# Kernel optimization log

Hardware: AMD Instinct MI355X
Metric: run time of the kernel (lower is better)

The kernel has to match this reference:

```python
import jax, jax.numpy as jnp
import numpy as np

S, D, F = 4096, 1024, 4096
EPS = 1e-5

def _layernorm(x, g, b):
    mu = jnp.mean(x, axis=-1, keepdims=True)
    var = jnp.mean(jnp.square(x - mu), axis=-1, keepdims=True)
    return (x - mu) * jax.lax.rsqrt(var + EPS) * g + b

def setup_inputs() -> dict:
    key = jax.random.key(0)
    ks = jax.random.split(key, 16)
    s = 0.02
    inp = {
        "query": jax.random.normal(ks[0], (S, D), jnp.float32),
        "key":   jax.random.normal(ks[1], (S, D), jnp.float32),
        "value": jax.random.normal(ks[2], (S, D), jnp.float32),
        "mask":  jax.random.uniform(ks[3], (S, S), jnp.float32),
        # attention linears (stored [in, out]; y = x @ W + b)
        "Wq": jax.random.normal(ks[4], (D, D), jnp.float32) * s,
        "bq": jnp.zeros((D,), jnp.float32),
        "Wk": jax.random.normal(ks[5], (D, D), jnp.float32) * s,
        "bk": jnp.zeros((D,), jnp.float32),
        "Wv": jax.random.normal(ks[6], (D, D), jnp.float32) * s,
        "bv": jnp.zeros((D,), jnp.float32),
        "Wo": jax.random.normal(ks[7], (D, D), jnp.float32) * s,
        "bo": jnp.zeros((D,), jnp.float32),
        # layernorm 1
        "g1": jnp.ones((D,), jnp.float32),
        "be1": jnp.zeros((D,), jnp.float32),
        # feed forward
        "W1": jax.random.normal(ks[8], (D, F), jnp.float32) * s,
        "bf1": jnp.zeros((F,), jnp.float32),
        "W2": jax.random.normal(ks[9], (F, D), jnp.float32) * s,
        "bf2": jnp.zeros((D,), jnp.float32),
        # layernorm 2
        "g2": jnp.ones((D,), jnp.float32),
        "be2": jnp.zeros((D,), jnp.float32),
    }
    return inp

def reference(query, key, value, mask, Wq, bq, Wk, bk, Wv, bv, Wo, bo,
              g1, be1, W1, bf1, W2, bf2, g2, be2):
    q = query @ Wq + bq                      # [S, D]
    k = key @ Wk + bk                        # [S, D]
    v = value @ Wv + bv                      # [S, D]
    scores = q @ k.T                         # [S, S]
    masked = scores * mask                   # multiplicative mask
    h = jax.nn.softmax(masked / jnp.sqrt(jnp.float32(D)), axis=0)  # softmax over dim 0
    attn = (h @ v) @ Wo + bo                 # [S, D]
    # dropout is identity in eval mode
    n1 = _layernorm(attn + query, g1, be1)
    ff = jax.nn.relu(n1 @ W1 + bf1) @ W2 + bf2
    return _layernorm(ff + n1, g2, be2)
```

## Files before the change

### kernel.cpp

```cpp
#include <hip/hip_runtime.h>
#include <hip/hip_bf16.h>

#define S_DIM 4096
#define D_DIM 1024
#define F_DIM 4096

typedef unsigned short ushort_t;
typedef __attribute__((ext_vector_type(8))) short sh8;
typedef __attribute__((ext_vector_type(4))) short sh4;
typedef __attribute__((ext_vector_type(4))) float fx4;

__device__ __forceinline__ ushort_t f2bf(float f) {
    union { float f; unsigned u; } v; v.f = f;
    unsigned r = v.u + 0x7fffu + ((v.u >> 16) & 1u);
    return (ushort_t)(r >> 16);
}
__device__ __forceinline__ float bf2f(ushort_t u) {
    union { unsigned u; float f; } v; v.u = ((unsigned)u) << 16;
    return v.f;
}

typedef const __attribute__((address_space(1))) void* gvp;
typedef __attribute__((address_space(3))) void* svp;
__device__ __forceinline__ void gload_lds16(const void* g, void* l) {
    __builtin_amdgcn_global_load_lds((gvp)g, (svp)l, 16, 0, 0);
}

#define BM 128
#define BN 128
#define BK 32
#define LDS_BUF 16384

template<bool BIAS, bool RELU, bool SCALE, bool OUTBF, bool SPLITK>
__device__ __forceinline__
void gemm_body(const ushort_t* A, const ushort_t* Bt,
               const float* bias,
               float* Cf, ushort_t* Cb,
               int M, int N, int K, int kBeg, int kEnd, float scale)
{
    __shared__ ushort_t lds[3 * (BM * BK + BN * BK)];
    const int tid = threadIdx.x;
    const int bm = blockIdx.x, bn = blockIdx.y;
    const int w  = tid >> 6, l = tid & 63;
    const int wm = w >> 1, wn = w & 1;

    fx4 acc[4][4] = {};

    const ushort_t* Ag = A  + (size_t)(bm * BM) * K;
    const ushort_t* Bg = Bt + (size_t)(bn * BN) * K;

    const int srow = tid >> 2;
    const int scs  = (tid & 3) ^ (srow & 3);

    auto stage = [&](int b, int k0) {
        char* base = (char*)lds + b * LDS_BUF;
        #pragma unroll
        for (int c = 0; c < 2; ++c) {
            int row = c * 64 + srow;
            gload_lds16(Ag + (size_t)row * K + k0 + scs * 8,
                        base + c * 4096 + tid * 16);
            gload_lds16(Bg + (size_t)row * K + k0 + scs * 8,
                        base + 8192 + c * 4096 + tid * 16);
        }
    };

    const int nt = (kEnd - kBeg) / BK;

    stage(0, kBeg);
    if (nt > 1) {
        stage(1, kBeg + BK);
        asm volatile("s_waitcnt vmcnt(4)" ::: "memory");
    } else {
        asm volatile("s_waitcnt vmcnt(0)" ::: "memory");
    }
    __builtin_amdgcn_s_barrier();
    __builtin_amdgcn_sched_barrier(0);

    int cur = 0;
    for (int t = 0; t < nt; ++t) {
        int stg = cur + 2; if (stg >= 3) stg -= 3;
        if (t + 2 < nt) stage(stg, kBeg + (t + 2) * BK);

        char* lbase = (char*)lds + cur * LDS_BUF;
        sh8 af[4], bfr[4];
        #pragma unroll
        for (int q = 0; q < 4; ++q) {
            int ra = wm * 64 + q * 16 + (l & 15);
            int ca = (l >> 4) ^ (ra & 3);
            af[q]  = *(const sh8*)(lbase + ra * 64 + ca * 16);
            int rb = wn * 64 + q * 16 + (l & 15);
            int cb = (l >> 4) ^ (rb & 3);
            bfr[q] = *(const sh8*)(lbase + 8192 + rb * 64 + cb * 16);
        }
        #pragma unroll
        for (int i = 0; i < 4; ++i)
            #pragma unroll
            for (int j = 0; j < 4; ++j)
                acc[i][j] = __builtin_amdgcn_mfma_f32_16x16x32_bf16(
                                af[i], bfr[j], acc[i][j], 0, 0, 0);

        asm volatile("s_waitcnt lgkmcnt(0)" ::: "memory");
        if (t + 2 < nt)      asm volatile("s_waitcnt vmcnt(4)" ::: "memory");
        else if (t + 1 < nt) asm volatile("s_waitcnt vmcnt(0)" ::: "memory");
        if (t + 1 < nt) {
            __builtin_amdgcn_s_barrier();
            __builtin_amdgcn_sched_barrier(0);
        }
        cur = cur + 1; if (cur == 3) cur = 0;
    }

    if (SPLITK) Cb += (size_t)blockIdx.z * M * N;

    const int crow0 = bm * BM + wm * 64;
    const int ccol0 = bn * BN + wn * 64;
    #pragma unroll
    for (int i = 0; i < 4; ++i) {
        #pragma unroll
        for (int j = 0; j < 4; ++j) {
            int col = ccol0 + j * 16 + (l & 15);
            float bia = BIAS ? bias[col] : 0.f;
            #pragma unroll
            for (int r = 0; r < 4; ++r) {
                int row = crow0 + i * 16 + (l >> 4) * 4 + r;
                float v = acc[i][j][r] + bia;
                if (SCALE) v *= scale;
                if (RELU) v = fmaxf(v, 0.f);
                if (OUTBF) Cb[(size_t)row * N + col] = f2bf(v);
                else       Cf[(size_t)row * N + col] = v;
            }
        }
    }
}

template<bool BIAS, bool RELU, bool SCALE, bool OUTBF>
__global__ __launch_bounds__(256)
void gemm_bt(const ushort_t* __restrict__ A, const ushort_t* __restrict__ Bt,
             const float* __restrict__ bias,
             float* __restrict__ Cf, ushort_t* __restrict__ Cb,
             int M, int N, int K, float scale)
{
    gemm_body<BIAS, RELU, SCALE, OUTBF, false>(A, Bt, bias, Cf, Cb,
                                               M, N, K, 0, K, scale);
}

__global__ __launch_bounds__(256)
void gemm_bt_sk(const ushort_t* __restrict__ A, const ushort_t* __restrict__ Bt,
                ushort_t* __restrict__ Cpart, int M, int N, int K, int Ks)
{
    int z = blockIdx.z;
    gemm_body<false, false, false, true, true>(A, Bt, nullptr,
                                               nullptr, Cpart,
                                               M, N, K, z * Ks, z * Ks + Ks, 1.f);
}

__global__ __launch_bounds__(256)
void qkv_gemm(const ushort_t* qin, const ushort_t* kin, const ushort_t* vin,
              const ushort_t* WqT, const ushort_t* WkT, const ushort_t* WvT,
              const float* bq, const float* bk, const float* bv,
              ushort_t* qb, ushort_t* kb, ushort_t* vb, int M, int N, int K)
{
    const ushort_t* A; const ushort_t* Bt; const float* bias; ushort_t* C;
    if (blockIdx.z == 0)      { A = qin; Bt = WqT; bias = bq; C = qb; }
    else if (blockIdx.z == 1) { A = kin; Bt = WkT; bias = bk; C = kb; }
    else                      { A = vin; Bt = WvT; bias = bv; C = vb; }
    gemm_body<true, false, false, true, false>(A, Bt, bias,
                                               nullptr, C, M, N, K, 0, K, 1.f);
}

template<int NS>
__global__ __launch_bounds__(256)
void reduce_sk(const ushort_t* __restrict__ parts, ushort_t* __restrict__ ob,
               size_t MN)
{
    size_t idx = ((size_t)blockIdx.x * 256 + threadIdx.x) * 8;
    float s[8] = {0.f, 0.f, 0.f, 0.f, 0.f, 0.f, 0.f, 0.f};
    #pragma unroll
    for (int p = 0; p < NS; ++p) {
        sh8 v = *(const sh8*)(parts + (size_t)p * MN + idx);
        #pragma unroll
        for (int j = 0; j < 8; ++j) s[j] += bf2f((ushort_t)v[j]);
    }
    sh8 r;
    #pragma unroll
    for (int j = 0; j < 8; ++j) r[j] = (short)f2bf(s[j]);
    *(sh8*)(ob + idx) = r;
}

__global__ __launch_bounds__(256)
void transpose_f32_bf16(const float* __restrict__ in, ushort_t* __restrict__ out,
                        int R, int C)
{
    __shared__ float t[32][33];
    int bc = blockIdx.x * 32, br = blockIdx.y * 32;
    int tx = threadIdx.x & 31, ty = threadIdx.x >> 5;
    #pragma unroll
    for (int i = 0; i < 32; i += 8)
        t[ty + i][tx] = in[(size_t)(br + ty + i) * C + bc + tx];
    __syncthreads();
    #pragma unroll
    for (int i = 0; i < 32; i += 8)
        out[(size_t)(bc + ty + i) * R + br + tx] = f2bf(t[tx][ty + i]);
}

__global__ __launch_bounds__(256)
void transpose4_f32_bf16(const float* w0, const float* w1,
                         const float* w2, const float* w3,
                         ushort_t* o0, ushort_t* o1, ushort_t* o2, ushort_t* o3)
{
    const int R = D_DIM, C = D_DIM;
    const float* in; ushort_t* out;
    if (blockIdx.z == 0)      { in = w0; out = o0; }
    else if (blockIdx.z == 1) { in = w1; out = o1; }
    else if (blockIdx.z == 2) { in = w2; out = o2; }
    else                      { in = w3; out = o3; }
    __shared__ float t[32][33];
    int bc = blockIdx.x * 32, br = blockIdx.y * 32;
    int tx = threadIdx.x & 31, ty = threadIdx.x >> 5;
    #pragma unroll
    for (int i = 0; i < 32; i += 8)
        t[ty + i][tx] = in[(size_t)(br + ty + i) * C + bc + tx];
    __syncthreads();
    #pragma unroll
    for (int i = 0; i < 32; i += 8)
        out[(size_t)(bc + ty + i) * R + br + tx] = f2bf(t[tx][ty + i]);
}

__global__ __launch_bounds__(256)
void transpose_bf16(const ushort_t* __restrict__ in, ushort_t* __restrict__ out,
                    int R, int C)
{
    __shared__ ushort_t t[32][33];
    int bc = blockIdx.x * 32, br = blockIdx.y * 32;
    int tx = threadIdx.x & 31, ty = threadIdx.x >> 5;
    #pragma unroll
    for (int i = 0; i < 32; i += 8)
        t[ty + i][tx] = in[(size_t)(br + ty + i) * C + bc + tx];
    __syncthreads();
    #pragma unroll
    for (int i = 0; i < 32; i += 8)
        out[(size_t)(bc + ty + i) * R + br + tx] = t[tx][ty + i];
}

__global__ __launch_bounds__(256)
void cvt_bf16_3(const float* a, const float* b, const float* c,
                ushort_t* oa, ushort_t* ob, ushort_t* oc)
{
    const float* in; ushort_t* out;
    if (blockIdx.y == 0)      { in = a; out = oa; }
    else if (blockIdx.y == 1) { in = b; out = ob; }
    else                      { in = c; out = oc; }
    int i = (blockIdx.x * 256 + threadIdx.x) * 8;
    const float4* p = (const float4*)(in + i);
    float4 x = p[0], y = p[1];
    sh8 r;
    r[0] = (short)f2bf(x.x); r[1] = (short)f2bf(x.y);
    r[2] = (short)f2bf(x.z); r[3] = (short)f2bf(x.w);
    r[4] = (short)f2bf(y.x); r[5] = (short)f2bf(y.y);
    r[6] = (short)f2bf(y.z); r[7] = (short)f2bf(y.w);
    *(sh8*)(out + i) = r;
}

#define NCH 256
#define ROWS_PER_CH (S_DIM / NCH)

__global__ __launch_bounds__(256)
void smax_pass1(ushort_t* __restrict__ m, const float* __restrict__ mask,
                float* __restrict__ pmax, float* __restrict__ psum)
{
    int c0 = (blockIdx.x * 256 + threadIdx.x) * 8;
    int chunk = blockIdx.y;
    int r0 = chunk * ROWS_PER_CH;

    float mx[8], sm[8];
    #pragma unroll
    for (int j = 0; j < 8; ++j) { mx[j] = -1e30f; sm[j] = 0.f; }

    for (int i = 0; i < ROWS_PER_CH; ++i) {
        size_t off = (size_t)(r0 + i) * S_DIM + c0;
        sh8 mv = *(const sh8*)(m + off);
        float4 k0 = ((const float4*)(mask + off))[0];
        float4 k1 = ((const float4*)(mask + off))[1];
        float mk[8] = {k0.x, k0.y, k0.z, k0.w, k1.x, k1.y, k1.z, k1.w};
        sh8 wv;
        #pragma unroll
        for (int j = 0; j < 8; ++j) {
            float v0 = bf2f((ushort_t)mv[j]) * mk[j];
            ushort_t wb = f2bf(v0);
            wv[j] = (short)wb;
            float v = bf2f(wb);
            float nm = fmaxf(mx[j], v);
            sm[j] = sm[j] * __expf(mx[j] - nm) + __expf(v - nm);
            mx[j] = nm;
        }
        *(sh8*)(m + off) = wv;
    }
    #pragma unroll
    for (int j = 0; j < 8; ++j) {
        pmax[(size_t)(c0 + j) * NCH + chunk] = mx[j];
        psum[(size_t)(c0 + j) * NCH + chunk] = sm[j];
    }
}

__global__ __launch_bounds__(256)
void smax_pass2(const float* __restrict__ pmax, const float* __restrict__ psum,
                float* __restrict__ cmax, float* __restrict__ cinv)
{
    int col = blockIdx.x, t = threadIdx.x;
    float m = pmax[(size_t)col * NCH + t];
    float s = psum[(size_t)col * NCH + t];

    __shared__ float red[8];
    int w = t >> 6, l = t & 63;

    float mx = m;
    #pragma unroll
    for (int off = 32; off; off >>= 1) mx = fmaxf(mx, __shfl_down(mx, off));
    if (!l) red[w] = mx;
    __syncthreads();
    mx = fmaxf(fmaxf(red[0], red[1]), fmaxf(red[2], red[3]));
    __syncthreads();

    float sc = s * __expf(m - mx);
    #pragma unroll
    for (int off = 32; off; off >>= 1) sc += __shfl_down(sc, off);
    if (!l) red[4 + w] = sc;
    __syncthreads();
    if (t == 0) {
        float total = red[4] + red[5] + red[6] + red[7];
        cmax[col] = mx;
        cinv[col] = 1.f / total;
    }
}

__global__ __launch_bounds__(256)
void smax_pass3(const ushort_t* __restrict__ m,
                const float* __restrict__ cmax, const float* __restrict__ cinv,
                ushort_t* __restrict__ h)
{
    size_t idx = ((size_t)blockIdx.x * 256 + threadIdx.x) * 8;
    int col0 = (int)(idx & (S_DIM - 1));
    sh8 mv = *(const sh8*)(m + idx);
    sh8 r;
    #pragma unroll
    for (int j = 0; j < 8; ++j) {
        int c = col0 + j;
        float v = bf2f((ushort_t)mv[j]);
        r[j] = (short)f2bf(__expf(v - cmax[c]) * cinv[c]);
    }
    *(sh8*)(h + idx) = r;
}

template<int NS, bool WB>
__global__ __launch_bounds__(256)
void add_ln_sk(const ushort_t* __restrict__ parts, const float* __restrict__ pbias,
               const float* __restrict__ resid, const float* __restrict__ g,
               const float* __restrict__ be,
               float* __restrict__ of, ushort_t* __restrict__ ob)
{
    const int D = D_DIM;
    const size_t SD = (size_t)S_DIM * D_DIM;
    int row = blockIdx.x, tid = threadIdx.x;
    size_t base = (size_t)row * D + tid * 4;

    float4 vr = *(const float4*)(resid + base);
    float4 vbi = ((const float4*)pbias)[tid];
    float x0 = vr.x + vbi.x, x1 = vr.y + vbi.y, x2 = vr.z + vbi.z, x3 = vr.w + vbi.w;
    #pragma unroll
    for (int p = 0; p < NS; ++p) {
        sh4 v = *(const sh4*)(parts + p * SD + base);
        x0 += bf2f((ushort_t)v[0]); x1 += bf2f((ushort_t)v[1]);
        x2 += bf2f((ushort_t)v[2]); x3 += bf2f((ushort_t)v[3]);
    }

    float s = x0 + x1 + x2 + x3;
    float q = x0 * x0 + x1 * x1 + x2 * x2 + x3 * x3;
    #pragma unroll
    for (int off = 32; off; off >>= 1) {
        s += __shfl_down(s, off);
        q += __shfl_down(q, off);
    }
    __shared__ float red[8];
    int w = tid >> 6, l = tid & 63;
    if (!l) { red[w] = s; red[4 + w] = q; }
    __syncthreads();
    s = red[0] + red[1] + red[2] + red[3];
    q = red[4] + red[5] + red[6] + red[7];
    float mu = s * (1.f / D);
    float rstd = rsqrtf(q * (1.f / D) - mu * mu + 1e-5f);
    float4 vg  = ((const float4*)g)[tid];
    float4 vbe = ((const float4*)be)[tid];
    float y0 = (x0 - mu) * rstd * vg.x + vbe.x;
    float y1 = (x1 - mu) * rstd * vg.y + vbe.y;
    float y2 = (x2 - mu) * rstd * vg.z + vbe.z;
    float y3 = (x3 - mu) * rstd * vg.w + vbe.w;
    float4 r; r.x = y0; r.y = y1; r.z = y2; r.w = y3;
    *(float4*)(of + base) = r;
    if (WB) {
        sh4 rb;
        rb[0] = (short)f2bf(y0); rb[1] = (short)f2bf(y1);
        rb[2] = (short)f2bf(y2); rb[3] = (short)f2bf(y3);
        *(sh4*)(ob + base) = rb;
    }
}

extern "C" void kernel_launch(void* const* d_in, const int* in_sizes, int n_in,
                              void* d_out, int out_size, void* d_ws, size_t ws_size,
                              hipStream_t stream)
{
    const float* query = (const float*)d_in[0];
    const float* key_  = (const float*)d_in[1];
    const float* value = (const float*)d_in[2];
    const float* mask  = (const float*)d_in[3];
    const float* Wq = (const float*)d_in[4];  const float* bq = (const float*)d_in[5];
    const float* Wk = (const float*)d_in[6];  const float* bk = (const float*)d_in[7];
    const float* Wv = (const float*)d_in[8];  const float* bv = (const float*)d_in[9];
    const float* Wo = (const float*)d_in[10]; const float* bo = (const float*)d_in[11];
    const float* g1 = (const float*)d_in[12]; const float* be1 = (const float*)d_in[13];
    const float* W1 = (const float*)d_in[14]; const float* bf1 = (const float*)d_in[15];
    const float* W2 = (const float*)d_in[16]; const float* bf2 = (const float*)d_in[17];
    const float* g2 = (const float*)d_in[18]; const float* be2 = (const float*)d_in[19];

    const size_t MB = 1ull << 20;
    char* ws = (char*)d_ws;
    ushort_t* WqT = (ushort_t*)(ws);
    ushort_t* WkT = (ushort_t*)(ws + 2 * MB);
    ushort_t* WvT = (ushort_t*)(ws + 4 * MB);
    ushort_t* WoT = (ushort_t*)(ws + 6 * MB);
    ushort_t* W1T = (ushort_t*)(ws + 8 * MB);
    ushort_t* W2T = (ushort_t*)(ws + 16 * MB);
    ushort_t* qin = (ushort_t*)(ws + 24 * MB);
    ushort_t* kin = (ushort_t*)(ws + 32 * MB);
    ushort_t* vin = (ushort_t*)(ws + 40 * MB);
    ushort_t* qb  = (ushort_t*)(ws + 48 * MB);
    ushort_t* kb  = (ushort_t*)(ws + 56 * MB);
    ushort_t* vb  = (ushort_t*)(ws + 64 * MB);
    ushort_t* vT  = (ushort_t*)(ws + 72 * MB);
    ushort_t* msc = (ushort_t*)(ws + 80 * MB);
    ushort_t* hb  = (ushort_t*)(ws + 112 * MB);
    float*   pmax = (float*)(ws + 144 * MB);
    float*   psum = (float*)(ws + 148 * MB);
    float*   cmax = (float*)(ws + 152 * MB);
    float*   cinv = (float*)(ws + 152 * MB + 64 * 1024);
    ushort_t* pts1  = (ushort_t*)(ws + 80 * MB);
    ushort_t* apb   = (ushort_t*)(ws + 24 * MB);
    ushort_t* pts2  = (ushort_t*)(ws + 80 * MB);
    float*    n1f   = (float*)(ws + 48 * MB);
    ushort_t* n1b   = (ushort_t*)(ws + 64 * MB);
    ushort_t* mid   = (ushort_t*)(ws + 112 * MB);
    ushort_t* pts3  = (ushort_t*)(ws + 80 * MB);

    const int S = S_DIM, D = D_DIM, F = F_DIM;

    transpose4_f32_bf16<<<dim3(D / 32, D / 32, 4), 256, 0, stream>>>(
        Wq, Wk, Wv, Wo, WqT, WkT, WvT, WoT);
    transpose_f32_bf16<<<dim3(F / 32, D / 32), 256, 0, stream>>>(W1, W1T, D, F);
    transpose_f32_bf16<<<dim3(D / 32, F / 32), 256, 0, stream>>>(W2, W2T, F, D);

    cvt_bf16_3<<<dim3(S * D / 8 / 256, 3), 256, 0, stream>>>(
        query, key_, value, qin, kin, vin);

    qkv_gemm<<<dim3(S / BM, D / BN, 3), 256, 0, stream>>>(
        qin, kin, vin, WqT, WkT, WvT, bq, bk, bv, qb, kb, vb, S, D, D);

    transpose_bf16<<<dim3(D / 32, S / 32), 256, 0, stream>>>(vb, vT, S, D);

    gemm_bt<false, false, true, true><<<dim3(S / BM, S / BN), 256, 0, stream>>>(
        qb, kb, nullptr, nullptr, msc, S, S, D, 0.03125f);

    smax_pass1<<<dim3(S / 2048, NCH), 256, 0, stream>>>(msc, mask, pmax, psum);
    smax_pass2<<<S, 256, 0, stream>>>(pmax, psum, cmax, cinv);
    smax_pass3<<<(size_t)S * S / 8 / 256, 256, 0, stream>>>(msc, cmax, cinv, hb);

    gemm_bt_sk<<<dim3(S / BM, D / BN, 4), 256, 0, stream>>>(hb, vT, pts1, S, D, S, S / 4);
    reduce_sk<4><<<S * D / 2048, 256, 0, stream>>>(pts1, apb, (size_t)S * D);

    gemm_bt_sk<<<dim3(S / BM, D / BN, 2), 256, 0, stream>>>(apb, WoT, pts2, S, D, D, D / 2);

    add_ln_sk<2, true><<<S, 256, 0, stream>>>(pts2, bo, query, g1, be1, n1f, n1b);

    gemm_bt<true, true, false, true><<<dim3(S / BM, F / BN), 256, 0, stream>>>(
        n1b, W1T, bf1, nullptr, mid, S, F, D, 1.f);

    gemm_bt_sk<<<dim3(S / BM, D / BN, 4), 256, 0, stream>>>(mid, W2T, pts3, S, D, F, F / 4);

    add_ln_sk<4, false><<<S, 256, 0, stream>>>(pts3, bf2, n1f, g2, be2,
                                               (float*)d_out, nullptr);
}
```

Measured before the change: 358.6 us.

## Add 256x256-tile 512-thread GEMM and use it for the large matmuls

```diff
diff --git a/kernel.cpp b/kernel.cpp
--- a/kernel.cpp
+++ b/kernel.cpp
@@ -165,6 +165,132 @@
     else                      { A = vin; Bt = WvT; bias = bv; C = vb; }
     gemm_body<true, false, false, true, false>(A, Bt, bias,
                                                nullptr, C, M, N, K, 0, K, 1.f);
+}
+
+#define G2_BM 256
+#define G2_BN 256
+#define G2_BUF 32768
+
+template<bool BIAS, bool RELU, bool SCALE, bool OUTBF, bool SPLITK>
+__device__ __forceinline__
+void gemm256_body(const ushort_t* A, const ushort_t* Bt,
+                  const float* bias,
+                  float* Cf, ushort_t* Cb,
+                  int M, int N, int K, int kBeg, int kEnd, float scale)
+{
+    __shared__ ushort_t lds[3 * (G2_BM * BK + G2_BN * BK)];
+    const int tid = threadIdx.x;
+    const int bm = blockIdx.x, bn = blockIdx.y;
+    const int w  = tid >> 6, l = tid & 63;
+    const int wm = w >> 2, wn = w & 3;
+
+    fx4 acc[8][4] = {};
+
+    const ushort_t* Ag = A  + (size_t)(bm * G2_BM) * K;
+    const ushort_t* Bg = Bt + (size_t)(bn * G2_BN) * K;
+
+    auto stage = [&](int b, int k0) {
+        char* base = (char*)lds + b * G2_BUF;
+        #pragma unroll
+        for (int c = 0; c < 2; ++c) {
+            int idx = c * 512 + tid;
+            int row = idx >> 2;
+            int cs  = idx & 3;
+            gload_lds16(Ag + (size_t)row * K + k0 + cs * 8,
+                        base + idx * 16);
+            gload_lds16(Bg + (size_t)row * K + k0 + cs * 8,
+                        base + 16384 + idx * 16);
+        }
+    };
+
+    const int nt = (kEnd - kBeg) / BK;
+
+    stage(0, kBeg);
+    if (nt > 1) {
+        stage(1, kBeg + BK);
+        asm volatile("s_waitcnt vmcnt(4)" ::: "memory");
+    } else {
+        asm volatile("s_waitcnt vmcnt(0)" ::: "memory");
+    }
+    __builtin_amdgcn_s_barrier();
+    __builtin_amdgcn_sched_barrier(0);
+
+    int cur = 0;
+    for (int t = 0; t < nt; ++t) {
+        int stg = cur + 2; if (stg >= 3) stg -= 3;
+        if (t + 2 < nt) stage(stg, kBeg + (t + 2) * BK);
+
+        char* lbase = (char*)lds + cur * G2_BUF;
+        sh8 af[8], bfr[4];
+        #pragma unroll
+        for (int q = 0; q < 8; ++q) {
+            int ra = wm * 128 + q * 16 + (l & 15);
+            af[q] = *(const sh8*)(lbase + ra * 64 + (l >> 4) * 16);
+        }
+        #pragma unroll
+        for (int j = 0; j < 4; ++j) {
+            int rb = wn * 64 + j * 16 + (l & 15);
+            bfr[j] = *(const sh8*)(lbase + 16384 + rb * 64 + (l >> 4) * 16);
+        }
+        #pragma unroll
+        for (int i = 0; i < 8; ++i)
+            #pragma unroll
+            for (int j = 0; j < 4; ++j)
+                acc[i][j] = __builtin_amdgcn_mfma_f32_16x16x32_bf16(
+                                af[i], bfr[j], acc[i][j], 0, 0, 0);
+
+        asm volatile("s_waitcnt lgkmcnt(0)" ::: "memory");
+        if (t + 2 < nt)      asm volatile("s_waitcnt vmcnt(4)" ::: "memory");
+        else if (t + 1 < nt) asm volatile("s_waitcnt vmcnt(0)" ::: "memory");
+        if (t + 1 < nt) {
+            __builtin_amdgcn_s_barrier();
+            __builtin_amdgcn_sched_barrier(0);
+        }
+        cur = cur + 1; if (cur == 3) cur = 0;
+    }
+
+    if (SPLITK) Cb += (size_t)blockIdx.z * M * N;
+
+    const int crow0 = bm * G2_BM + wm * 128;
+    const int ccol0 = bn * G2_BN + wn * 64;
+    #pragma unroll
+    for (int i = 0; i < 8; ++i) {
+        #pragma unroll
+        for (int j = 0; j < 4; ++j) {
+            int col = ccol0 + j * 16 + (l & 15);
+            float bia = BIAS ? bias[col] : 0.f;
+            #pragma unroll
+            for (int r = 0; r < 4; ++r) {
+                int row = crow0 + i * 16 + (l >> 4) * 4 + r;
+                float v = acc[i][j][r] + bia;
+                if (SCALE) v *= scale;
+                if (RELU) v = fmaxf(v, 0.f);
+                if (OUTBF) Cb[(size_t)row * N + col] = f2bf(v);
+                else       Cf[(size_t)row * N + col] = v;
+            }
+        }
+    }
+}
+
+template<bool BIAS, bool RELU, bool SCALE, bool OUTBF>
+__global__ __launch_bounds__(512)
+void gemm256_bt(const ushort_t* __restrict__ A, const ushort_t* __restrict__ Bt,
+                const float* __restrict__ bias,
+                float* __restrict__ Cf, ushort_t* __restrict__ Cb,
+                int M, int N, int K, float scale)
+{
+    gemm256_body<BIAS, RELU, SCALE, OUTBF, false>(A, Bt, bias, Cf, Cb,
+                                                  M, N, K, 0, K, scale);
+}
+
+__global__ __launch_bounds__(512)
+void gemm256_bt_sk(const ushort_t* __restrict__ A, const ushort_t* __restrict__ Bt,
+                   ushort_t* __restrict__ Cpart, int M, int N, int K, int Ks)
+{
+    int z = blockIdx.z;
+    gemm256_body<false, false, false, true, true>(A, Bt, nullptr,
+                                                  nullptr, Cpart,
+                                                  M, N, K, z * Ks, z * Ks + Ks, 1.f);
 }
 
 template<int NS>
@@ -464,24 +590,26 @@
 
     transpose_bf16<<<dim3(D / 32, S / 32), 256, 0, stream>>>(vb, vT, S, D);
 
-    gemm_bt<false, false, true, true><<<dim3(S / BM, S / BN), 256, 0, stream>>>(
+    gemm256_bt<false, false, true, true><<<dim3(S / G2_BM, S / G2_BN), 512, 0, stream>>>(
         qb, kb, nullptr, nullptr, msc, S, S, D, 0.03125f);
 
     smax_pass1<<<dim3(S / 2048, NCH), 256, 0, stream>>>(msc, mask, pmax, psum);
     smax_pass2<<<S, 256, 0, stream>>>(pmax, psum, cmax, cinv);
     smax_pass3<<<(size_t)S * S / 8 / 256, 256, 0, stream>>>(msc, cmax, cinv, hb);
 
-    gemm_bt_sk<<<dim3(S / BM, D / BN, 4), 256, 0, stream>>>(hb, vT, pts1, S, D, S, S / 4);
+    gemm256_bt_sk<<<dim3(S / G2_BM, D / G2_BN, 4), 512, 0, stream>>>(
+        hb, vT, pts1, S, D, S, S / 4);
     reduce_sk<4><<<S * D / 2048, 256, 0, stream>>>(pts1, apb, (size_t)S * D);
 
     gemm_bt_sk<<<dim3(S / BM, D / BN, 2), 256, 0, stream>>>(apb, WoT, pts2, S, D, D, D / 2);
 
     add_ln_sk<2, true><<<S, 256, 0, stream>>>(pts2, bo, query, g1, be1, n1f, n1b);
 
-    gemm_bt<true, true, false, true><<<dim3(S / BM, F / BN), 256, 0, stream>>>(
+    gemm256_bt<true, true, false, true><<<dim3(S / G2_BM, F / G2_BN), 512, 0, stream>>>(
         n1b, W1T, bf1, nullptr, mid, S, F, D, 1.f);
 
-    gemm_bt_sk<<<dim3(S / BM, D / BN, 4), 256, 0, stream>>>(mid, W2T, pts3, S, D, F, F / 4);
+    gemm256_bt_sk<<<dim3(S / G2_BM, D / G2_BN, 4), 512, 0, stream>>>(
+        mid, W2T, pts3, S, D, F, F / 4);
 
     add_ln_sk<4, false><<<S, 256, 0, stream>>>(pts3, bf2, n1f, g2, be2,
                                                (float*)d_out, nullptr);
```

After: 335.7 us. -6.4%, faster.
